# Kernel optimization log

Measured on AMD Instinct MI355X. Metric: run time of the kernel, lower is better.

The kernel has to match this reference:

```python
import jax, jax.numpy as jnp
import numpy as np

N_NODES = 20000
N_EDGES = 320000
X_DIM = 128
EDGE_DIM = 64
HIDDEN = 256
OUT_DIM = 256
LAYERS = 3
N_GRAPHS = 64


def setup_inputs() -> dict:
    key = jax.random.key(0)
    ks = jax.random.split(key, 20)
    x = jax.random.normal(ks[0], (N_NODES, X_DIM), dtype=jnp.float32)
    edge_index = jax.random.randint(ks[1], (2, N_EDGES), 0, N_NODES, dtype=jnp.int64)
    edge_attr = jax.random.normal(ks[2], (N_EDGES, EDGE_DIM), dtype=jnp.float32)
    batch_ids = jnp.sort(jax.random.randint(ks[3], (N_NODES,), 0, N_GRAPHS, dtype=jnp.int64))

    def lin(k, fan_in, fan_out):
        bound = 1.0 / np.sqrt(fan_in)
        kw, kb = jax.random.split(k)
        W = jax.random.uniform(kw, (fan_in, fan_out), minval=-bound, maxval=bound, dtype=jnp.float32)
        b = jax.random.uniform(kb, (fan_out,), minval=-bound, maxval=bound, dtype=jnp.float32)
        return W, b

    xproj_W, xproj_b = lin(ks[4], X_DIM, HIDDEN)
    edge_W, edge_b, mlp_W1, mlp_b1, mlp_W2, mlp_b2 = [], [], [], [], [], []
    for l in range(LAYERS):
        eW, eb = lin(ks[5 + l], EDGE_DIM, HIDDEN)
        w1, b1 = lin(ks[8 + l], HIDDEN, HIDDEN)
        w2, b2 = lin(ks[11 + l], HIDDEN, HIDDEN)
        edge_W.append(eW); edge_b.append(eb)
        mlp_W1.append(w1); mlp_b1.append(b1)
        mlp_W2.append(w2); mlp_b2.append(b2)
    out_W1, out_b1 = lin(ks[14], HIDDEN, HIDDEN)
    out_W2, out_b2 = lin(ks[15], HIDDEN, OUT_DIM)
    return {
        "x": x, "edge_index": edge_index, "edge_attr": edge_attr, "batch_ids": batch_ids,
        "xproj_W": xproj_W, "xproj_b": xproj_b,
        "edge_W": jnp.stack(edge_W), "edge_b": jnp.stack(edge_b),
        "mlp_W1": jnp.stack(mlp_W1), "mlp_b1": jnp.stack(mlp_b1),
        "mlp_W2": jnp.stack(mlp_W2), "mlp_b2": jnp.stack(mlp_b2),
        "out_W1": out_W1, "out_b1": out_b1, "out_W2": out_W2, "out_b2": out_b2,
    }


def reference(x, edge_index, edge_attr, batch_ids, xproj_W, xproj_b,
              edge_W, edge_b, mlp_W1, mlp_b1, mlp_W2, mlp_b2,
              out_W1, out_b1, out_W2, out_b2):
    src, dst = edge_index[0], edge_index[1]
    h = x @ xproj_W + xproj_b  # [N, H]
    for l in range(LAYERS):
        # GINE message: relu(x_j + Lin(edge_attr)), aggregated by sum at target
        msg = jax.nn.relu(h[src] + edge_attr @ edge_W[l] + edge_b[l])  # [E, H]
        agg = jax.ops.segment_sum(msg, dst, num_segments=N_NODES)      # [N, H]
        z = h + agg  # (1 + eps) * x_i with eps = 0
        z = jax.nn.relu(z @ mlp_W1[l] + mlp_b1[l]) @ mlp_W2[l] + mlp_b2[l]
        h = jax.nn.relu(z)  # outer F.relu in forward
    # global mean pool over graphs
    sums = jax.ops.segment_sum(h, batch_ids, num_segments=N_GRAPHS)    # [G, H]
    counts = jax.ops.segment_sum(jnp.ones((h.shape[0],), h.dtype), batch_ids, num_segments=N_GRAPHS)
    g = sums / jnp.maximum(counts, 1.0)[:, None]
    g = jax.nn.relu(g @ out_W1 + out_b1) @ out_W2 + out_b2
    # F.normalize(dim=-1): x / max(||x||_2, eps)
    norm = jnp.maximum(jnp.linalg.norm(g, axis=-1, keepdims=True), 1e-12)
    return g / norm
```

## Files before the change

### kernel.cpp

```cpp
#include <hip/hip_runtime.h>

#define N_NODES 20000
#define N_EDGES 320000
#define X_DIM 128
#define EDGE_DIM 64
#define HIDDEN 256
#define N_GRAPHS 64
#define LAYERS 3

#define NPB 8
#define EB 32
#define ET 4
#define PSPLIT 8
#define NBLK ((N_NODES + 255) / 256)

typedef __attribute__((ext_vector_type(8))) short short8;
typedef __attribute__((ext_vector_type(4))) float floatx4;

__device__ __forceinline__ unsigned short f2bf(float f) {
    union { float f; unsigned u; } v; v.f = f;
    return (unsigned short)((v.u + 0x7FFFu + ((v.u >> 16) & 1u)) >> 16);
}
__device__ __forceinline__ float bf2f(unsigned short u) {
    return __uint_as_float(((unsigned)u) << 16);
}


__global__ __launch_bounds__(256) void deg_kernel(const int* __restrict__ ei,
                                                  int* __restrict__ deg)
{
    int e = blockIdx.x * 256 + threadIdx.x;
    if (e < N_EDGES) atomicAdd(&deg[ei[N_EDGES + e]], 1);
}

__global__ __launch_bounds__(256) void pscan_kernel(const int* __restrict__ deg,
                                                    int* __restrict__ rp,
                                                    int* __restrict__ bsum)
{
    __shared__ int buf[256];
    const int t = threadIdx.x;
    const int i = blockIdx.x * 256 + t;
    int v = (i < N_NODES) ? deg[i] : 0;
    buf[t] = v;
    __syncthreads();
    for (int off = 1; off < 256; off <<= 1) {
        int a = (t >= off) ? buf[t - off] : 0;
        __syncthreads();
        buf[t] += a;
        __syncthreads();
    }
    if (i < N_NODES) rp[i] = buf[t] - v;
    if (t == 255) bsum[blockIdx.x] = buf[255];
}

__global__ __launch_bounds__(128) void bscan_kernel(const int* __restrict__ bsum,
                                                    int* __restrict__ boff)
{
    __shared__ int buf[128];
    const int t = threadIdx.x;
    int v = (t < NBLK) ? bsum[t] : 0;
    buf[t] = v;
    __syncthreads();
    for (int off = 1; off < 128; off <<= 1) {
        int a = (t >= off) ? buf[t - off] : 0;
        __syncthreads();
        buf[t] += a;
        __syncthreads();
    }
    if (t < NBLK) boff[t] = buf[t] - v;
}

__global__ __launch_bounds__(256) void addoff_kernel(int* __restrict__ rp,
                                                     const int* __restrict__ boff)
{
    const int i = blockIdx.x * 256 + threadIdx.x;
    if (i < N_NODES) rp[i] += boff[blockIdx.x];
    if (i == 0) rp[N_NODES] = N_EDGES;
}

__global__ __launch_bounds__(256) void scatter_kernel(const int* __restrict__ ei,
                                                      const int* __restrict__ rp,
                                                      int* __restrict__ cursor,
                                                      int* __restrict__ perm)
{
    const int e = blockIdx.x * 256 + threadIdx.x;
    if (e < N_EDGES) {
        const int d = ei[N_EDGES + e];
        const int pos = atomicAdd(&cursor[d], 1);
        perm[rp[d] + pos] = e;
    }
}

__global__ __launch_bounds__(256) void permute_kernel(
    const float* __restrict__ ea, const int* __restrict__ ei,
    const int* __restrict__ perm, unsigned short* __restrict__ eab,
    int* __restrict__ srcs, int* __restrict__ dsts)
{
    const int tid = blockIdx.x * 256 + threadIdx.x;
    const int e = tid >> 3, seg = tid & 7;
    const int p = perm[e];
    const float* sp = ea + (size_t)p * EDGE_DIM + seg * 8;
    const float4 v0 = *(const float4*)sp;
    const float4 v1 = *(const float4*)(sp + 4);
    short8 o;
    o[0] = (short)f2bf(v0.x); o[1] = (short)f2bf(v0.y);
    o[2] = (short)f2bf(v0.z); o[3] = (short)f2bf(v0.w);
    o[4] = (short)f2bf(v1.x); o[5] = (short)f2bf(v1.y);
    o[6] = (short)f2bf(v1.z); o[7] = (short)f2bf(v1.w);
    *(short8*)(eab + (size_t)e * EDGE_DIM + seg * 8) = o;
    if (seg == 0) { srcs[e] = ei[p]; dsts[e] = ei[N_EDGES + p]; }
}

__global__ __launch_bounds__(256) void swizzle_kernel(const float* __restrict__ W,
                                                      unsigned short* __restrict__ out,
                                                      int KK)
{
    const int i = blockIdx.x * 256 + threadIdx.x;
    if (i >= 8192 * KK) return;
    const int j = i & 7, lane = (i >> 3) & 63, rem = i >> 9;
    const int kk = rem % KK, rem2 = rem / KK, nt = rem2 & 3, wvv = rem2 >> 2;
    const int n = wvv * 64 + nt * 16 + (lane & 15);
    const int k = kk * 32 + (lane >> 4) * 8 + j;
    out[i] = f2bf(W[k * HIDDEN + n]);
}


__global__ __launch_bounds__(256) void node_proj_kernel(
    const float* __restrict__ x, const float* __restrict__ W,
    const float* __restrict__ b, float* __restrict__ h,
    unsigned short* __restrict__ hbf, float* __restrict__ z)
{
    const int t = threadIdx.x;
    const int row0 = blockIdx.x * NPB;
    __shared__ float xs[NPB][X_DIM];
    for (int idx = t; idx < NPB * X_DIM; idx += 256)
        xs[idx / X_DIM][idx % X_DIM] = x[(size_t)row0 * X_DIM + idx];
    __syncthreads();
    float acc[NPB];
    const float bt = b[t];
#pragma unroll
    for (int r = 0; r < NPB; r++) acc[r] = bt;
    for (int k = 0; k < X_DIM; k++) {
        const float wv = W[k * HIDDEN + t];
#pragma unroll
        for (int r = 0; r < NPB; r++) acc[r] += xs[r][k] * wv;
    }
#pragma unroll
    for (int r = 0; r < NPB; r++) {
        const size_t idx = (size_t)(row0 + r) * HIDDEN + t;
        h[idx] = acc[r];
        hbf[idx] = f2bf(acc[r]);
        z[idx] = 0.f;
    }
}

__global__ __launch_bounds__(256) void edge_mfma_kernel(
    const unsigned short* __restrict__ eab, const int* __restrict__ srcs,
    const int* __restrict__ dsts, const unsigned short* __restrict__ Ws,
    const float* __restrict__ b, const unsigned short* __restrict__ hbf,
    float* __restrict__ z)
{
    const int t = threadIdx.x;
    const int lane = t & 63, wv = t >> 6, q = lane >> 4, m15 = lane & 15;
    __shared__ unsigned short msg[EB][264];
    __shared__ int s_src[2][EB], s_dst[2][EB];

    short8 bfr[4][2];
#pragma unroll
    for (int nt = 0; nt < 4; nt++)
#pragma unroll
        for (int kk = 0; kk < 2; kk++)
            bfr[nt][kk] = *(const short8*)(Ws + ((((wv * 4 + nt) * 2 + kk) * 64) + lane) * 8);
    const float bt = b[t];

    if (t < EB) {
        const int e0 = blockIdx.x * ET * EB;
        s_src[0][t] = srcs[e0 + t];
        s_dst[0][t] = dsts[e0 + t];
    }
    __syncthreads();

    float s = 0.f;
    int prev = s_dst[0][0];

    for (int tile = 0; tile < ET; tile++) {
        const int cur = tile & 1;
        const int e0 = (blockIdx.x * ET + tile) * EB;

        unsigned short hv[EB];
#pragma unroll
        for (int e = 0; e < EB; e++)
            hv[e] = hbf[(size_t)s_src[cur][e] * HIDDEN + t];

        if (tile + 1 < ET && t < EB) {
            s_src[1 - cur][t] = srcs[e0 + EB + t];
            s_dst[1 - cur][t] = dsts[e0 + EB + t];
        }

        floatx4 acc[2][4];
#pragma unroll
        for (int mt = 0; mt < 2; mt++)
#pragma unroll
            for (int nt = 0; nt < 4; nt++)
                acc[mt][nt] = (floatx4){0.f, 0.f, 0.f, 0.f};
#pragma unroll
        for (int kk = 0; kk < 2; kk++) {
            const short8 a0 = *(const short8*)(eab + (size_t)(e0 + m15) * EDGE_DIM + kk * 32 + q * 8);
            const short8 a1 = *(const short8*)(eab + (size_t)(e0 + 16 + m15) * EDGE_DIM + kk * 32 + q * 8);
#pragma unroll
            for (int nt = 0; nt < 4; nt++) {
                acc[0][nt] = __builtin_amdgcn_mfma_f32_16x16x32_bf16(a0, bfr[nt][kk], acc[0][nt], 0, 0, 0);
                acc[1][nt] = __builtin_amdgcn_mfma_f32_16x16x32_bf16(a1, bfr[nt][kk], acc[1][nt], 0, 0, 0);
            }
        }
#pragma unroll
        for (int mt = 0; mt < 2; mt++)
#pragma unroll
            for (int nt = 0; nt < 4; nt++)
#pragma unroll
                for (int r = 0; r < 4; r++)
                    msg[mt * 16 + q * 4 + r][wv * 64 + nt * 16 + m15] = f2bf(acc[mt][nt][r]);
        __syncthreads();

#pragma unroll
        for (int e = 0; e < EB; e++) {
            const int d = s_dst[cur][e];
            if (d != prev) {
                atomicAdd(&z[(size_t)prev * HIDDEN + t], s);
                s = 0.f; prev = d;
            }
            const float m = bf2f(msg[e][t]) + bt + bf2f(hv[e]);
            s += m > 0.f ? m : 0.f;
        }
        __syncthreads();
    }
    atomicAdd(&z[(size_t)prev * HIDDEN + t], s);
}

__global__ __launch_bounds__(256) void mlp_mfma_kernel(
    const unsigned short* __restrict__ W1s, const float* __restrict__ b1,
    const unsigned short* __restrict__ W2s, const float* __restrict__ b2,
    float* __restrict__ h, float* __restrict__ z, unsigned short* __restrict__ hbf)
{
    const int t = threadIdx.x;
    const int lane = t & 63, wv = t >> 6, q = lane >> 4, m15 = lane & 15;
    const int row0 = blockIdx.x * 32;
    __shared__ __align__(16) unsigned short zs[32][264];

#pragma unroll
    for (int r = 0; r < 32; r++) {
        const size_t idx = (size_t)(row0 + r) * HIDDEN + t;
        zs[r][t] = f2bf(h[idx] + z[idx]);
        z[idx] = 0.f;
    }
    __syncthreads();

    float b1v[4], b2v[4];
#pragma unroll
    for (int nt = 0; nt < 4; nt++) {
        const int c = wv * 64 + nt * 16 + m15;
        b1v[nt] = b1[c]; b2v[nt] = b2[c];
    }

    floatx4 acc[2][4];
#pragma unroll
    for (int mt = 0; mt < 2; mt++)
#pragma unroll
        for (int nt = 0; nt < 4; nt++)
            acc[mt][nt] = (floatx4){0.f, 0.f, 0.f, 0.f};

#pragma unroll
    for (int kk = 0; kk < 8; kk++) {
        short8 bfr[4];
#pragma unroll
        for (int nt = 0; nt < 4; nt++)
            bfr[nt] = *(const short8*)(W1s + ((((wv * 4 + nt) * 8 + kk) * 64) + lane) * 8);
        const short8 a0 = *(const short8*)&zs[m15][kk * 32 + q * 8];
        const short8 a1 = *(const short8*)&zs[16 + m15][kk * 32 + q * 8];
#pragma unroll
        for (int nt = 0; nt < 4; nt++) {
            acc[0][nt] = __builtin_amdgcn_mfma_f32_16x16x32_bf16(a0, bfr[nt], acc[0][nt], 0, 0, 0);
            acc[1][nt] = __builtin_amdgcn_mfma_f32_16x16x32_bf16(a1, bfr[nt], acc[1][nt], 0, 0, 0);
        }
    }
    __syncthreads();
#pragma unroll
    for (int mt = 0; mt < 2; mt++)
#pragma unroll
        for (int nt = 0; nt < 4; nt++)
#pragma unroll
            for (int r = 0; r < 4; r++) {
                const int row = mt * 16 + q * 4 + r, c = wv * 64 + nt * 16 + m15;
                const float v = acc[mt][nt][r] + b1v[nt];
                zs[row][c] = f2bf(v > 0.f ? v : 0.f);
            }
    __syncthreads();

#pragma unroll
    for (int mt = 0; mt < 2; mt++)
#pragma unroll
        for (int nt = 0; nt < 4; nt++)
            acc[mt][nt] = (floatx4){0.f, 0.f, 0.f, 0.f};

#pragma unroll
    for (int kk = 0; kk < 8; kk++) {
        short8 bfr[4];
#pragma unroll
        for (int nt = 0; nt < 4; nt++)
            bfr[nt] = *(const short8*)(W2s + ((((wv * 4 + nt) * 8 + kk) * 64) + lane) * 8);
        const short8 a0 = *(const short8*)&zs[m15][kk * 32 + q * 8];
        const short8 a1 = *(const short8*)&zs[16 + m15][kk * 32 + q * 8];
#pragma unroll
        for (int nt = 0; nt < 4; nt++) {
            acc[0][nt] = __builtin_amdgcn_mfma_f32_16x16x32_bf16(a0, bfr[nt], acc[0][nt], 0, 0, 0);
            acc[1][nt] = __builtin_amdgcn_mfma_f32_16x16x32_bf16(a1, bfr[nt], acc[1][nt], 0, 0, 0);
        }
    }
#pragma unroll
    for (int mt = 0; mt < 2; mt++)
#pragma unroll
        for (int nt = 0; nt < 4; nt++)
#pragma unroll
            for (int r = 0; r < 4; r++) {
                const int row = mt * 16 + q * 4 + r, c = wv * 64 + nt * 16 + m15;
                float v = acc[mt][nt][r] + b2v[nt];
                v = v > 0.f ? v : 0.f;
                const size_t idx = (size_t)(row0 + row) * HIDDEN + c;
                h[idx] = v;
                hbf[idx] = f2bf(v);
            }
}

__global__ __launch_bounds__(256) void pool_kernel(
    const float* __restrict__ h, const int* __restrict__ bid,
    float* __restrict__ gsum)
{
    const int g = blockIdx.x / PSPLIT;
    const int part = blockIdx.x % PSPLIT;
    const int t = threadIdx.x;
    int lo = 0, hi = N_NODES;
    while (lo < hi) { int mid = (lo + hi) >> 1; if (bid[mid] < g) lo = mid + 1; else hi = mid; }
    const int start = lo;
    hi = N_NODES;
    while (lo < hi) { int mid = (lo + hi) >> 1; if (bid[mid] < g + 1) lo = mid + 1; else hi = mid; }
    const int end = lo;
    const int len = end - start;
    const int chunk = (len + PSPLIT - 1) / PSPLIT;
    const int s0 = start + part * chunk;
    const int s1 = min(s0 + chunk, end);
    if (s0 >= s1) return;
    float s = 0.f;
    for (int i = s0; i < s1; i++) s += h[(size_t)i * HIDDEN + t];
    atomicAdd(&gsum[g * HIDDEN + t], s);
}

__global__ __launch_bounds__(256) void head_kernel(
    const float* __restrict__ gsum, const int* __restrict__ bid,
    const float* __restrict__ W1, const float* __restrict__ b1,
    const float* __restrict__ W2, const float* __restrict__ b2,
    float* __restrict__ out)
{
    const int g = blockIdx.x;
    const int t = threadIdx.x;
    __shared__ float gs[HIDDEN];
    __shared__ float t1[HIDDEN];
    __shared__ float red[256];
    int lo = 0, hi = N_NODES;
    while (lo < hi) { int mid = (lo + hi) >> 1; if (bid[mid] < g) lo = mid + 1; else hi = mid; }
    const int start = lo;
    hi = N_NODES;
    while (lo < hi) { int mid = (lo + hi) >> 1; if (bid[mid] < g + 1) lo = mid + 1; else hi = mid; }
    float cnt = (float)(lo - start);
    cnt = cnt > 1.f ? cnt : 1.f;
    gs[t] = gsum[g * HIDDEN + t] / cnt;
    __syncthreads();
    float acc = b1[t];
    for (int k = 0; k < HIDDEN; k++) acc += gs[k] * W1[k * HIDDEN + t];
    t1[t] = acc > 0.f ? acc : 0.f;
    __syncthreads();
    float acc2 = b2[t];
    for (int k = 0; k < HIDDEN; k++) acc2 += t1[k] * W2[k * HIDDEN + t];
    red[t] = acc2 * acc2;
    __syncthreads();
    for (int s = 128; s > 0; s >>= 1) {
        if (t < s) red[t] += red[t + s];
        __syncthreads();
    }
    float norm = sqrtf(red[0]);
    norm = norm > 1e-12f ? norm : 1e-12f;
    out[g * HIDDEN + t] = acc2 / norm;
}

extern "C" void kernel_launch(void* const* d_in, const int* in_sizes, int n_in,
                              void* d_out, int out_size, void* d_ws, size_t ws_size,
                              hipStream_t stream)
{
    const float* x   = (const float*)d_in[0];
    const int*   ei  = (const int*)d_in[1];
    const float* ea  = (const float*)d_in[2];
    const int*   bid = (const int*)d_in[3];
    const float* xW  = (const float*)d_in[4];
    const float* xb  = (const float*)d_in[5];
    const float* eW  = (const float*)d_in[6];
    const float* eb  = (const float*)d_in[7];
    const float* W1  = (const float*)d_in[8];
    const float* b1  = (const float*)d_in[9];
    const float* W2  = (const float*)d_in[10];
    const float* b2  = (const float*)d_in[11];
    const float* oW1 = (const float*)d_in[12];
    const float* ob1 = (const float*)d_in[13];
    const float* oW2 = (const float*)d_in[14];
    const float* ob2 = (const float*)d_in[15];
    float* out = (float*)d_out;

    char* p = (char*)d_ws;
    auto alloc = [&](size_t bytes) { char* r = p; p += (bytes + 255) & ~(size_t)255; return r; };
    float* h     = (float*)alloc((size_t)N_NODES * HIDDEN * 4);
    float* z     = (float*)alloc((size_t)N_NODES * HIDDEN * 4);
    float* gpool = (float*)alloc((size_t)N_GRAPHS * HIDDEN * 4);
    int* deg     = (int*)alloc(N_NODES * 4);
    int* rowptr  = (int*)alloc((N_NODES + 1) * 4);
    int* cursor  = (int*)alloc(N_NODES * 4);
    int* bsum    = (int*)alloc(NBLK * 4);
    int* boff    = (int*)alloc(NBLK * 4);
    int* perm    = (int*)alloc((size_t)N_EDGES * 4);
    int* srcs    = (int*)alloc((size_t)N_EDGES * 4);
    int* dsts    = (int*)alloc((size_t)N_EDGES * 4);
    unsigned short* hbf = (unsigned short*)alloc((size_t)N_NODES * HIDDEN * 2);
    unsigned short* eab = (unsigned short*)alloc((size_t)N_EDGES * EDGE_DIM * 2);
    unsigned short* eWs = (unsigned short*)alloc((size_t)LAYERS * EDGE_DIM * HIDDEN * 2);
    unsigned short* W1s = (unsigned short*)alloc((size_t)LAYERS * HIDDEN * HIDDEN * 2);
    unsigned short* W2s = (unsigned short*)alloc((size_t)LAYERS * HIDDEN * HIDDEN * 2);

    hipMemsetAsync(deg, 0, N_NODES * sizeof(int), stream);
    hipMemsetAsync(cursor, 0, N_NODES * sizeof(int), stream);
    hipMemsetAsync(gpool, 0, N_GRAPHS * HIDDEN * sizeof(float), stream);
    deg_kernel<<<(N_EDGES + 255) / 256, 256, 0, stream>>>(ei, deg);
    pscan_kernel<<<NBLK, 256, 0, stream>>>(deg, rowptr, bsum);
    bscan_kernel<<<1, 128, 0, stream>>>(bsum, boff);
    addoff_kernel<<<NBLK, 256, 0, stream>>>(rowptr, boff);
    scatter_kernel<<<(N_EDGES + 255) / 256, 256, 0, stream>>>(ei, rowptr, cursor, perm);
    permute_kernel<<<(N_EDGES * 8) / 256, 256, 0, stream>>>(ea, ei, perm, eab, srcs, dsts);
    for (int l = 0; l < LAYERS; l++) {
        swizzle_kernel<<<64, 256, 0, stream>>>(eW + (size_t)l * EDGE_DIM * HIDDEN,
                                               eWs + (size_t)l * EDGE_DIM * HIDDEN, 2);
        swizzle_kernel<<<256, 256, 0, stream>>>(W1 + (size_t)l * HIDDEN * HIDDEN,
                                                W1s + (size_t)l * HIDDEN * HIDDEN, 8);
        swizzle_kernel<<<256, 256, 0, stream>>>(W2 + (size_t)l * HIDDEN * HIDDEN,
                                                W2s + (size_t)l * HIDDEN * HIDDEN, 8);
    }

    node_proj_kernel<<<N_NODES / NPB, 256, 0, stream>>>(x, xW, xb, h, hbf, z);
    for (int l = 0; l < LAYERS; l++) {
        edge_mfma_kernel<<<N_EDGES / (EB * ET), 256, 0, stream>>>(
            eab, srcs, dsts, eWs + (size_t)l * EDGE_DIM * HIDDEN,
            eb + l * HIDDEN, hbf, z);
        mlp_mfma_kernel<<<N_NODES / 32, 256, 0, stream>>>(
            W1s + (size_t)l * HIDDEN * HIDDEN, b1 + l * HIDDEN,
            W2s + (size_t)l * HIDDEN * HIDDEN, b2 + l * HIDDEN, h, z, hbf);
    }
    pool_kernel<<<N_GRAPHS * PSPLIT, 256, 0, stream>>>(h, bid, gpool);
    head_kernel<<<N_GRAPHS, 256, 0, stream>>>(gpool, bid, oW1, ob1, oW2, ob2, out);
}
```

Measured before the change: 600.4 us.

## Consolidate preprocessing launches, fuse weight swizzles, double edge tiles per block

Replaces the three-kernel prefix scan with a single-block scan, merges nine per-layer weight swizzle launches into one kernel, and coalesces three memsets into one contiguous memset. It also raises the edge kernel's tiles per block from 4 to 8 and skips zeroing z after the last layer. The goal is less launch overhead and redundant memory traffic. The single-block scan is serial per thread, and the larger edge tile halves the block count, which may reduce parallelism.

New measurement: 616.1 us. 2.6% more time.

```diff
diff --git a/kernel.cpp b/kernel.cpp
--- a/kernel.cpp
+++ b/kernel.cpp
@@ -10,9 +10,11 @@
 
 #define NPB 8
 #define EB 32
-#define ET 4
+#define ET 8
 #define PSPLIT 8
-#define NBLK ((N_NODES + 255) / 256)
+#define SWZ_E (EDGE_DIM * HIDDEN)
+#define SWZ_W (HIDDEN * HIDDEN)
+#define SWZ_PER_LAYER (SWZ_E + 2 * SWZ_W)
 
 typedef __attribute__((ext_vector_type(8))) short short8;
 typedef __attribute__((ext_vector_type(4))) float floatx4;
@@ -33,49 +35,30 @@
     if (e < N_EDGES) atomicAdd(&deg[ei[N_EDGES + e]], 1);
 }
 
-__global__ __launch_bounds__(256) void pscan_kernel(const int* __restrict__ deg,
-                                                    int* __restrict__ rp,
-                                                    int* __restrict__ bsum)
-{
-    __shared__ int buf[256];
-    const int t = threadIdx.x;
-    const int i = blockIdx.x * 256 + t;
-    int v = (i < N_NODES) ? deg[i] : 0;
-    buf[t] = v;
-    __syncthreads();
+__global__ __launch_bounds__(256) void scan_kernel(const int* __restrict__ deg,
+                                                   int* __restrict__ rp)
+{
+    __shared__ int part[256];
+    const int t = threadIdx.x;
+    const int i0 = t * 79;
+    const int i1 = min(i0 + 79, N_NODES);
+    int s = 0;
+    for (int i = i0; i < i1; i++) s += deg[i];
+    part[t] = s;
+    __syncthreads();
+    int v = part[t];
     for (int off = 1; off < 256; off <<= 1) {
-        int a = (t >= off) ? buf[t - off] : 0;
+        int a = (t >= off) ? part[t - off] : 0;
         __syncthreads();
-        buf[t] += a;
+        part[t] += a;
         __syncthreads();
     }
-    if (i < N_NODES) rp[i] = buf[t] - v;
-    if (t == 255) bsum[blockIdx.x] = buf[255];
-}
-
-__global__ __launch_bounds__(128) void bscan_kernel(const int* __restrict__ bsum,
-                                                    int* __restrict__ boff)
-{
-    __shared__ int buf[128];
-    const int t = threadIdx.x;
-    int v = (t < NBLK) ? bsum[t] : 0;
-    buf[t] = v;
-    __syncthreads();
-    for (int off = 1; off < 128; off <<= 1) {
-        int a = (t >= off) ? buf[t - off] : 0;
-        __syncthreads();
-        buf[t] += a;
-        __syncthreads();
-    }
-    if (t < NBLK) boff[t] = buf[t] - v;
-}
-
-__global__ __launch_bounds__(256) void addoff_kernel(int* __restrict__ rp,
-                                                     const int* __restrict__ boff)
-{
-    const int i = blockIdx.x * 256 + threadIdx.x;
-    if (i < N_NODES) rp[i] += boff[blockIdx.x];
-    if (i == 0) rp[N_NODES] = N_EDGES;
+    int run = part[t] - v;
+    for (int i = i0; i < i1; i++) {
+        rp[i] = run;
+        run += deg[i];
+    }
+    if (t == 0) rp[N_NODES] = N_EDGES;
 }
 
 __global__ __launch_bounds__(256) void scatter_kernel(const int* __restrict__ ei,
@@ -111,17 +94,27 @@
     if (seg == 0) { srcs[e] = ei[p]; dsts[e] = ei[N_EDGES + p]; }
 }
 
-__global__ __launch_bounds__(256) void swizzle_kernel(const float* __restrict__ W,
-                                                      unsigned short* __restrict__ out,
-                                                      int KK)
+__global__ __launch_bounds__(256) void swizzle_all_kernel(
+    const float* __restrict__ eW, const float* __restrict__ W1,
+    const float* __restrict__ W2, unsigned short* __restrict__ eWs,
+    unsigned short* __restrict__ W1s, unsigned short* __restrict__ W2s)
 {
     const int i = blockIdx.x * 256 + threadIdx.x;
-    if (i >= 8192 * KK) return;
-    const int j = i & 7, lane = (i >> 3) & 63, rem = i >> 9;
+    if (i >= LAYERS * SWZ_PER_LAYER) return;
+    const int l = i / SWZ_PER_LAYER, r = i % SWZ_PER_LAYER;
+    const float* W; unsigned short* out; int KK, base;
+    if (r < SWZ_E) {
+        W = eW + (size_t)l * SWZ_E; out = eWs + (size_t)l * SWZ_E; KK = 2; base = r;
+    } else if (r < SWZ_E + SWZ_W) {
+        W = W1 + (size_t)l * SWZ_W; out = W1s + (size_t)l * SWZ_W; KK = 8; base = r - SWZ_E;
+    } else {
+        W = W2 + (size_t)l * SWZ_W; out = W2s + (size_t)l * SWZ_W; KK = 8; base = r - SWZ_E - SWZ_W;
+    }
+    const int j = base & 7, lane = (base >> 3) & 63, rem = base >> 9;
     const int kk = rem % KK, rem2 = rem / KK, nt = rem2 & 3, wvv = rem2 >> 2;
     const int n = wvv * 64 + nt * 16 + (lane & 15);
     const int k = kk * 32 + (lane >> 4) * 8 + j;
-    out[i] = f2bf(W[k * HIDDEN + n]);
+    out[base] = f2bf(W[k * HIDDEN + n]);
 }
 
 
@@ -240,7 +233,8 @@
 __global__ __launch_bounds__(256) void mlp_mfma_kernel(
     const unsigned short* __restrict__ W1s, const float* __restrict__ b1,
     const unsigned short* __restrict__ W2s, const float* __restrict__ b2,
-    float* __restrict__ h, float* __restrict__ z, unsigned short* __restrict__ hbf)
+    float* __restrict__ h, float* __restrict__ z, unsigned short* __restrict__ hbf,
+    int zero_z)
 {
     const int t = threadIdx.x;
     const int lane = t & 63, wv = t >> 6, q = lane >> 4, m15 = lane & 15;
@@ -251,7 +245,7 @@
     for (int r = 0; r < 32; r++) {
         const size_t idx = (size_t)(row0 + r) * HIDDEN + t;
         zs[r][t] = f2bf(h[idx] + z[idx]);
-        z[idx] = 0.f;
+        if (zero_z) z[idx] = 0.f;
     }
     __syncthreads();
 
@@ -419,45 +413,34 @@
     float* z     = (float*)alloc((size_t)N_NODES * HIDDEN * 4);
     float* gpool = (float*)alloc((size_t)N_GRAPHS * HIDDEN * 4);
     int* deg     = (int*)alloc(N_NODES * 4);
+    int* cursor  = (int*)alloc(N_NODES * 4);
     int* rowptr  = (int*)alloc((N_NODES + 1) * 4);
-    int* cursor  = (int*)alloc(N_NODES * 4);
-    int* bsum    = (int*)alloc(NBLK * 4);
-    int* boff    = (int*)alloc(NBLK * 4);
     int* perm    = (int*)alloc((size_t)N_EDGES * 4);
     int* srcs    = (int*)alloc((size_t)N_EDGES * 4);
     int* dsts    = (int*)alloc((size_t)N_EDGES * 4);
     unsigned short* hbf = (unsigned short*)alloc((size_t)N_NODES * HIDDEN * 2);
     unsigned short* eab = (unsigned short*)alloc((size_t)N_EDGES * EDGE_DIM * 2);
-    unsigned short* eWs = (unsigned short*)alloc((size_t)LAYERS * EDGE_DIM * HIDDEN * 2);
-    unsigned short* W1s = (unsigned short*)alloc((size_t)LAYERS * HIDDEN * HIDDEN * 2);
-    unsigned short* W2s = (unsigned short*)alloc((size_t)LAYERS * HIDDEN * HIDDEN * 2);
-
-    hipMemsetAsync(deg, 0, N_NODES * sizeof(int), stream);
-    hipMemsetAsync(cursor, 0, N_NODES * sizeof(int), stream);
-    hipMemsetAsync(gpool, 0, N_GRAPHS * HIDDEN * sizeof(float), stream);
+    unsigned short* eWs = (unsigned short*)alloc((size_t)LAYERS * SWZ_E * 2);
+    unsigned short* W1s = (unsigned short*)alloc((size_t)LAYERS * SWZ_W * 2);
+    unsigned short* W2s = (unsigned short*)alloc((size_t)LAYERS * SWZ_W * 2);
+
+    hipMemsetAsync(gpool, 0, (size_t)((char*)rowptr - (char*)gpool), stream);
     deg_kernel<<<(N_EDGES + 255) / 256, 256, 0, stream>>>(ei, deg);
-    pscan_kernel<<<NBLK, 256, 0, stream>>>(deg, rowptr, bsum);
-    bscan_kernel<<<1, 128, 0, stream>>>(bsum, boff);
-    addoff_kernel<<<NBLK, 256, 0, stream>>>(rowptr, boff);
+    scan_kernel<<<1, 256, 0, stream>>>(deg, rowptr);
     scatter_kernel<<<(N_EDGES + 255) / 256, 256, 0, stream>>>(ei, rowptr, cursor, perm);
     permute_kernel<<<(N_EDGES * 8) / 256, 256, 0, stream>>>(ea, ei, perm, eab, srcs, dsts);
-    for (int l = 0; l < LAYERS; l++) {
-        swizzle_kernel<<<64, 256, 0, stream>>>(eW + (size_t)l * EDGE_DIM * HIDDEN,
-                                               eWs + (size_t)l * EDGE_DIM * HIDDEN, 2);
-        swizzle_kernel<<<256, 256, 0, stream>>>(W1 + (size_t)l * HIDDEN * HIDDEN,
-                                                W1s + (size_t)l * HIDDEN * HIDDEN, 8);
-        swizzle_kernel<<<256, 256, 0, stream>>>(W2 + (size_t)l * HIDDEN * HIDDEN,
-                                                W2s + (size_t)l * HIDDEN * HIDDEN, 8);
-    }
+    swizzle_all_kernel<<<(LAYERS * SWZ_PER_LAYER + 255) / 256, 256, 0, stream>>>(
+        eW, W1, W2, eWs, W1s, W2s);
 
     node_proj_kernel<<<N_NODES / NPB, 256, 0, stream>>>(x, xW, xb, h, hbf, z);
     for (int l = 0; l < LAYERS; l++) {
         edge_mfma_kernel<<<N_EDGES / (EB * ET), 256, 0, stream>>>(
-            eab, srcs, dsts, eWs + (size_t)l * EDGE_DIM * HIDDEN,
+            eab, srcs, dsts, eWs + (size_t)l * SWZ_E,
             eb + l * HIDDEN, hbf, z);
         mlp_mfma_kernel<<<N_NODES / 32, 256, 0, stream>>>(
-            W1s + (size_t)l * HIDDEN * HIDDEN, b1 + l * HIDDEN,
-            W2s + (size_t)l * HIDDEN * HIDDEN, b2 + l * HIDDEN, h, z, hbf);
+            W1s + (size_t)l * SWZ_W, b1 + l * HIDDEN,
+            W2s + (size_t)l * SWZ_W, b2 + l * HIDDEN, h, z, hbf,
+            l + 1 < LAYERS ? 1 : 0);
     }
     pool_kernel<<<N_GRAPHS * PSPLIT, 256, 0, stream>>>(h, bid, gpool);
     head_kernel<<<N_GRAPHS, 256, 0, stream>>>(gpool, bid, oW1, ob1, oW2, ob2, out);
```
